# Performance work log

Hardware: AMD Instinct MI355X
Metric: run time of the kernel (lower is better)

The kernel has to match this reference:

```python
import jax, jax.numpy as jnp
import numpy as np
import math

B, L, D = 4, 4096, 64

def setup_inputs() -> dict:
    key = jax.random.key(0)
    kq, kk, kv = jax.random.split(key, 3)
    q = jax.random.normal(kq, (B, L, D), dtype=jnp.float32)
    k = jax.random.normal(kk, (B, L, D), dtype=jnp.float32)
    v = jax.random.normal(kv, (B, L, D), dtype=jnp.float32)
    return {"q": q, "k": k, "v": v}

def reference(q, k, v):
    d_model = k.shape[-1]
    # score[b,i,j] = <q_i, k_j> / sqrt(d)   -> [B, L, L]
    score = jnp.einsum('bid,bjd->bij', q, k) / math.sqrt(d_model)
    attn = jax.nn.softmax(score.astype(jnp.float32), axis=-1)
    # Faithful to source: output = (v^T @ attn)^T = attn^T @ v
    # output[b,j,d] = sum_i attn[b,i,j] * v[b,i,d]
    out = jnp.einsum('bij,bid->bjd', attn, v)
    return out
```

## Files before the change

### kernel.cpp

```cpp
#include <hip/hip_runtime.h>
#include <hip/hip_bf16.h>

#define LQ 4096
#define DD 64
#define NB 4
#define NTOT ((size_t)NB * LQ * DD)
#define NROW ((size_t)NB * LQ)

typedef __attribute__((ext_vector_type(4))) float f32x4;
typedef __attribute__((ext_vector_type(8))) short short8;
typedef __attribute__((ext_vector_type(4))) short short4v;
typedef __attribute__((ext_vector_type(2))) unsigned int uint2v;
typedef __attribute__((ext_vector_type(4))) unsigned short ushort4v;

static __device__ __forceinline__ unsigned short f2bf(float x) {
  __hip_bfloat16 h = __float2bfloat16(x);
  return __builtin_bit_cast(unsigned short, h);
}
static __device__ __forceinline__ float bf2f(unsigned short u) {
  unsigned int v = ((unsigned int)u) << 16;
  return __builtin_bit_cast(float, v);
}
static __device__ __forceinline__ float ex2(float x) { return __builtin_amdgcn_exp2f(x); }

static __device__ __forceinline__ f32x4 mfma16(short4v a, short4v b, f32x4 c) {
#if __has_builtin(__builtin_amdgcn_mfma_f32_16x16x16bf16_1k)
  return __builtin_amdgcn_mfma_f32_16x16x16bf16_1k(a, b, c, 0, 0, 0);
#else
  asm volatile("v_mfma_f32_16x16x16_bf16 %0, %1, %2, %0"
               : "+v"(c) : "v"(a), "v"(b));
  return c;
#endif
}

static __device__ __forceinline__ void gl_lds16(const unsigned short* g, unsigned short* l) {
  __builtin_amdgcn_global_load_lds(
      (const __attribute__((address_space(1))) unsigned int*)g,
      (__attribute__((address_space(3))) unsigned int*)l, 16, 0, 0);
}

#define C1 0.18033688011112042f

__global__ __launch_bounds__(256) void prep_kernel(
    const float* __restrict__ q, const float* __restrict__ k,
    const float* __restrict__ v,
    unsigned short* __restrict__ Qb, unsigned short* __restrict__ Kb,
    unsigned short* __restrict__ Vb)
{
  const int arr = blockIdx.x >> 9;
  const size_t off = (((size_t)(blockIdx.x & 511)) * 256 + threadIdx.x) * 8;
  const float* s = arr == 0 ? q : arr == 1 ? k : v;
  unsigned short* d = arr == 0 ? Qb : arr == 1 ? Kb : Vb;
  const f32x4 x0 = *(const f32x4*)(s + off);
  const f32x4 x1 = *(const f32x4*)(s + off + 4);
  ushort4v o0 = { f2bf(x0[0]), f2bf(x0[1]), f2bf(x0[2]), f2bf(x0[3]) };
  ushort4v o1 = { f2bf(x1[0]), f2bf(x1[1]), f2bf(x1[2]), f2bf(x1[3]) };
  *(ushort4v*)(d + off) = o0;
  *(ushort4v*)(d + off + 4) = o1;
}

__global__ __launch_bounds__(256, 2) void stats_kernel(
    const unsigned short* __restrict__ Qb, const unsigned short* __restrict__ Kb,
    float* __restrict__ part_ls)
{
  __shared__ __align__(16) unsigned short stK[3][2048];
  const int bx = blockIdx.x;
  const int jc = bx & 7, it = (bx >> 3) & 15, b = bx >> 7;
  const int tid = threadIdx.x, w = tid >> 6, lane = tid & 63;
  const int l15 = lane & 15, g = lane >> 4;
  const int i0 = it * 256 + w * 64;
  const int jbase = jc * 512;
  const unsigned short* Kbase = Kb + (size_t)b * LQ * DD;

  short8 aq[4][2];
#pragma unroll
  for (int is = 0; is < 4; ++is)
#pragma unroll
    for (int kh = 0; kh < 2; ++kh)
      aq[is][kh] = *(const short8*)(Qb + ((size_t)b * LQ + i0 + is * 16 + l15) * DD + kh * 32 + g * 8);

  float ls[4][4];
#pragma unroll
  for (int is = 0; is < 4; ++is)
#pragma unroll
    for (int qq = 0; qq < 4; ++qq) ls[is][qq] = 0.f;

  const int srow = w * 8 + (lane >> 3);
  const int scol = ((lane & 7) ^ (lane >> 3)) << 3;

  gl_lds16(Kbase + (size_t)(jbase + srow) * DD + scol, &stK[0][w * 512]);
  gl_lds16(Kbase + (size_t)(jbase + 32 + srow) * DD + scol, &stK[1][w * 512]);
  asm volatile("s_waitcnt vmcnt(1)" ::: "memory");
  __builtin_amdgcn_s_barrier();

  for (int itr = 0; itr < 16; ++itr) {
    const int cur = itr % 3;
    const int tn = (itr + 2 < 16) ? itr + 2 : 15;
    gl_lds16(Kbase + (size_t)(jbase + tn * 32 + srow) * DD + scol, &stK[(itr + 2) % 3][w * 512]);

    short8 kf[2][2];
#pragma unroll
    for (int jsub = 0; jsub < 2; ++jsub)
#pragma unroll
      for (int kh = 0; kh < 2; ++kh) {
        const int row = jsub * 16 + l15;
        kf[jsub][kh] = *(const short8*)(&stK[cur][row * 64 + (((kh * 4 + g) ^ (l15 & 7)) << 3)]);
      }
#pragma unroll
    for (int is = 0; is < 4; ++is)
#pragma unroll
      for (int jsub = 0; jsub < 2; ++jsub) {
        f32x4 tt = __builtin_amdgcn_mfma_f32_16x16x32_bf16(
            aq[is][0], kf[jsub][0], (f32x4){0.f, 0.f, 0.f, 0.f}, 0, 0, 0);
        tt = __builtin_amdgcn_mfma_f32_16x16x32_bf16(aq[is][1], kf[jsub][1], tt, 0, 0, 0);
#pragma unroll
        for (int qq = 0; qq < 4; ++qq) ls[is][qq] += ex2(tt[qq] * C1);
      }
    asm volatile("s_waitcnt vmcnt(1)" ::: "memory");
    __builtin_amdgcn_s_barrier();
  }
#pragma unroll
  for (int mask = 1; mask <= 8; mask <<= 1)
#pragma unroll
    for (int is = 0; is < 4; ++is)
#pragma unroll
      for (int qq = 0; qq < 4; ++qq) ls[is][qq] += __shfl_xor(ls[is][qq], mask, 64);
  if (l15 == 0) {
#pragma unroll
    for (int is = 0; is < 4; ++is)
#pragma unroll
      for (int qq = 0; qq < 4; ++qq)
        part_ls[(size_t)jc * NROW + b * LQ + i0 + is * 16 + g * 4 + qq] = ls[is][qq];
  }
}

__global__ __launch_bounds__(256) void combine_kernel(
    const float* __restrict__ part_ls, const unsigned short* __restrict__ Vb,
    unsigned short* __restrict__ Vs)
{
  const size_t base = ((size_t)blockIdx.x * 256 + threadIdx.x) * 8;
  const int r = (int)(base >> 6);
  float l = 0.f;
#pragma unroll
  for (int jc = 0; jc < 8; ++jc) l += part_ls[(size_t)jc * NROW + r];
  const float s = 1.0f / l;
  const ushort4v a = *(const ushort4v*)(Vb + base);
  const ushort4v c = *(const ushort4v*)(Vb + base + 4);
  ushort4v oa = { f2bf(bf2f(a[0]) * s), f2bf(bf2f(a[1]) * s),
                  f2bf(bf2f(a[2]) * s), f2bf(bf2f(a[3]) * s) };
  ushort4v oc = { f2bf(bf2f(c[0]) * s), f2bf(bf2f(c[1]) * s),
                  f2bf(bf2f(c[2]) * s), f2bf(bf2f(c[3]) * s) };
  *(ushort4v*)(Vs + base) = oa;
  *(ushort4v*)(Vs + base + 4) = oc;
}

__global__ __launch_bounds__(1024, 4) void attn_out_kernel(
    const unsigned short* __restrict__ Qb, const unsigned short* __restrict__ Kb,
    const unsigned short* __restrict__ Vs, float* __restrict__ out)
{
  __shared__ __align__(16) unsigned short stage[16][2][2048];

  const int bx = blockIdx.x;
  const int jt = bx & 63;
  const int b  = bx >> 6;
  const int tid = threadIdx.x, w = tid >> 6, lane = tid & 63;
  const int p = w >> 1, sub = w & 1;
  const int l15 = lane & 15, g = lane >> 4;
  const int j0 = jt * 64 + sub * 32;

  const unsigned short* Qbase = Qb + (size_t)b * LQ * DD;
  const unsigned short* Vbase = Vs + (size_t)b * LQ * DD;

  short8 ka[2][2];
#pragma unroll
  for (int jsl = 0; jsl < 2; ++jsl)
#pragma unroll
    for (int kh = 0; kh < 2; ++kh)
      ka[jsl][kh] = *(const short8*)(Kb + ((size_t)b * LQ + j0 + jsl * 16 + l15) * DD + kh * 32 + g * 8);

  f32x4 acc[2][4];
#pragma unroll
  for (int jsl = 0; jsl < 2; ++jsl)
#pragma unroll
    for (int ds = 0; ds < 4; ++ds) acc[jsl][ds] = (f32x4){0.f, 0.f, 0.f, 0.f};

  const int ibase = p * 512;
  const int qrow = lane >> 3;
  const int qcol = ((lane & 7) ^ (lane >> 3)) << 3;
  const int vgr = ((lane & 31) >> 3) * 4 + ((lane >> 1) & 3);
  const int vdc = (lane >> 5) * 16 + (lane & 1) * 8;

  const unsigned sbyte = (unsigned)(size_t)&stage[w][0][0];

#define STAGE(BUF, I0) do { \
    _Pragma("unroll") \
    for (int kk = 0; kk < 2; ++kk) { \
      gl_lds16(Qbase + (size_t)((I0) + kk * 8 + qrow) * DD + qcol, &stage[w][BUF][kk * 512]); \
      gl_lds16(Vbase + (size_t)((I0) + vgr) * DD + kk * 32 + vdc, &stage[w][BUF][1024 + kk * 512]); \
    } \
  } while (0)

  STAGE(0, ibase);
  STAGE(1, ibase + 16);

  for (int itr = 0; itr < 32; ++itr) {
    const int cur = itr & 1;
    if (itr < 31) asm volatile("s_waitcnt vmcnt(4)" ::: "memory");
    else          asm volatile("s_waitcnt vmcnt(0)" ::: "memory");

    short8 qf[2];
#pragma unroll
    for (int kh = 0; kh < 2; ++kh)
      qf[kh] = *(const short8*)(&stage[w][cur][l15 * 64 + (((kh * 4 + g) ^ (l15 & 7)) << 3)]);

    unsigned long long v0, v1, v2, v3;
    const unsigned av = sbyte + cur * 4096 + 2048 + g * 128 + l15 * 8;
    asm volatile(
        "ds_read_b64_tr_b16 %0, %4\n\t"
        "ds_read_b64_tr_b16 %1, %4 offset:512\n\t"
        "ds_read_b64_tr_b16 %2, %4 offset:1024\n\t"
        "ds_read_b64_tr_b16 %3, %4 offset:1536\n\t"
        "s_waitcnt lgkmcnt(0)"
        : "=&v"(v0), "=&v"(v1), "=&v"(v2), "=&v"(v3)
        : "v"(av) : "memory");
    short4v vf[4];
    vf[0] = __builtin_bit_cast(short4v, v0);
    vf[1] = __builtin_bit_cast(short4v, v1);
    vf[2] = __builtin_bit_cast(short4v, v2);
    vf[3] = __builtin_bit_cast(short4v, v3);

    if (itr + 2 < 32) STAGE(cur, ibase + (itr + 2) * 16);

    __builtin_amdgcn_s_setprio(1);
#pragma unroll
    for (int jsl = 0; jsl < 2; ++jsl) {
      f32x4 tt = __builtin_amdgcn_mfma_f32_16x16x32_bf16(
          qf[0], ka[jsl][0], (f32x4){0.f, 0.f, 0.f, 0.f}, 0, 0, 0);
      tt = __builtin_amdgcn_mfma_f32_16x16x32_bf16(qf[1], ka[jsl][1], tt, 0, 0, 0);
      const unsigned a0 = __builtin_bit_cast(unsigned, ex2(tt[0] * C1)) + 0x8000u;
      const unsigned a1 = __builtin_bit_cast(unsigned, ex2(tt[1] * C1)) + 0x8000u;
      const unsigned a2 = __builtin_bit_cast(unsigned, ex2(tt[2] * C1)) + 0x8000u;
      const unsigned a3 = __builtin_bit_cast(unsigned, ex2(tt[3] * C1)) + 0x8000u;
      uint2v uu;
      uu[0] = __builtin_amdgcn_perm(a1, a0, 0x07060302u);
      uu[1] = __builtin_amdgcn_perm(a3, a2, 0x07060302u);
      const short4v pa = __builtin_bit_cast(short4v, uu);
      acc[jsl][0] = mfma16(pa, vf[0], acc[jsl][0]);
      acc[jsl][1] = mfma16(pa, vf[1], acc[jsl][1]);
      acc[jsl][2] = mfma16(pa, vf[2], acc[jsl][2]);
      acc[jsl][3] = mfma16(pa, vf[3], acc[jsl][3]);
    }
    __builtin_amdgcn_s_setprio(0);
  }
#undef STAGE

  __syncthreads();
  float* red = (float*)&stage[0][0][0];
#pragma unroll
  for (int jsl = 0; jsl < 2; ++jsl)
#pragma unroll
    for (int ds = 0; ds < 4; ++ds)
#pragma unroll
      for (int qq = 0; qq < 4; ++qq)
        red[w * 2048 + (jsl * 16 + g * 4 + qq) * 64 + ds * 16 + l15] = acc[jsl][ds][qq];
  __syncthreads();
  {
    float* op = out + ((size_t)b * LQ + jt * 64) * DD;
#pragma unroll
    for (int rr = 0; rr < 4; ++rr) {
      const int r = w * 4 + rr;
      const int sr = r >> 5, rl = r & 31;
      float s = 0.f;
#pragma unroll
      for (int pp = 0; pp < 8; ++pp)
        s += red[(pp * 2 + sr) * 2048 + rl * 64 + lane];
      op[r * 64 + lane] = s;
    }
  }
}

extern "C" void kernel_launch(void* const* d_in, const int* in_sizes, int n_in,
                              void* d_out, int out_size, void* d_ws, size_t ws_size,
                              hipStream_t stream) {
  const float* q = (const float*)d_in[0];
  const float* k = (const float*)d_in[1];
  const float* v = (const float*)d_in[2];

  unsigned short* Qb = (unsigned short*)d_ws;
  unsigned short* Kb = Qb + NTOT;
  unsigned short* Vb = Kb + NTOT;
  unsigned short* Vs = Vb + NTOT;
  float* part_ls = (float*)(Vs + NTOT);
  float* outp = (float*)d_out;

  prep_kernel<<<1536, 256, 0, stream>>>(q, k, v, Qb, Kb, Vb);
  stats_kernel<<<NB * 16 * 8, 256, 0, stream>>>(Qb, Kb, part_ls);
  combine_kernel<<<512, 256, 0, stream>>>(part_ls, Vb, Vs);
  attn_out_kernel<<<NB * 64, 1024, 0, stream>>>(Qb, Kb, Vs, outp);
}
```

Measured before the change: 60.80 us.

## Pre-swizzle Q/K/V into MFMA fragment layout and load directly to registers

The prep and combine kernels now write Q, K and scaled V in a fragment-major layout, so each lane's MFMA operand is one contiguous 16-byte global load. The stats and attention kernels drop the LDS staging, swizzling and transpose reads, and prefetch fragments straight into registers with a 3-deep ring. V is now read from fp32 and scaled in combine, which removes a separate bf16 V copy. Stats uses 16 j-chunks and both main kernels remap block indices to interleave batches. The cost is more registers held per wave, with no LDS reuse of Q/V across the waves of a block.

```diff
diff --git a/kernel.cpp b/kernel.cpp
--- a/kernel.cpp
+++ b/kernel.cpp
@@ -6,6 +6,7 @@
 #define NB 4
 #define NTOT ((size_t)NB * LQ * DD)
 #define NROW ((size_t)NB * LQ)
+#define NJC 16
 
 typedef __attribute__((ext_vector_type(4))) float f32x4;
 typedef __attribute__((ext_vector_type(8))) short short8;
@@ -16,10 +17,6 @@
 static __device__ __forceinline__ unsigned short f2bf(float x) {
   __hip_bfloat16 h = __float2bfloat16(x);
   return __builtin_bit_cast(unsigned short, h);
-}
-static __device__ __forceinline__ float bf2f(unsigned short u) {
-  unsigned int v = ((unsigned int)u) << 16;
-  return __builtin_bit_cast(float, v);
 }
 static __device__ __forceinline__ float ex2(float x) { return __builtin_amdgcn_exp2f(x); }
 
@@ -33,91 +30,105 @@
 #endif
 }
 
-static __device__ __forceinline__ void gl_lds16(const unsigned short* g, unsigned short* l) {
-  __builtin_amdgcn_global_load_lds(
-      (const __attribute__((address_space(1))) unsigned int*)g,
-      (__attribute__((address_space(3))) unsigned int*)l, 16, 0, 0);
-}
-
 #define C1 0.18033688011112042f
+
 
 __global__ __launch_bounds__(256) void prep_kernel(
     const float* __restrict__ q, const float* __restrict__ k,
-    const float* __restrict__ v,
-    unsigned short* __restrict__ Qb, unsigned short* __restrict__ Kb,
-    unsigned short* __restrict__ Vb)
+    unsigned short* __restrict__ Qf, unsigned short* __restrict__ Kf)
 {
-  const int arr = blockIdx.x >> 9;
-  const size_t off = (((size_t)(blockIdx.x & 511)) * 256 + threadIdx.x) * 8;
-  const float* s = arr == 0 ? q : arr == 1 ? k : v;
-  unsigned short* d = arr == 0 ? Qb : arr == 1 ? Kb : Vb;
-  const f32x4 x0 = *(const f32x4*)(s + off);
-  const f32x4 x1 = *(const f32x4*)(s + off + 4);
-  ushort4v o0 = { f2bf(x0[0]), f2bf(x0[1]), f2bf(x0[2]), f2bf(x0[3]) };
-  ushort4v o1 = { f2bf(x1[0]), f2bf(x1[1]), f2bf(x1[2]), f2bf(x1[3]) };
-  *(ushort4v*)(d + off) = o0;
-  *(ushort4v*)(d + off + 4) = o1;
-}
-
-__global__ __launch_bounds__(256, 2) void stats_kernel(
-    const unsigned short* __restrict__ Qb, const unsigned short* __restrict__ Kb,
+  __shared__ __align__(16) unsigned short tile[64][72];
+  const int bx = blockIdx.x;
+  const int b = bx >> 6, s = bx & 63;
+  const int tid = threadIdx.x;
+  const int r = tid >> 2, c0 = (tid & 3) << 4;
+  const int w = tid >> 6, lane = tid & 63;
+  const int l15 = lane & 15, g = lane >> 4;
+  const size_t rowbase = ((size_t)b * LQ + s * 64 + r) * DD + c0;
+  const size_t bbase = (size_t)b * LQ * DD;
+
+#pragma unroll
+  for (int arr = 0; arr < 2; ++arr) {
+    const float* src = arr ? k : q;
+    unsigned short* dst = arr ? Kf : Qf;
+    ushort4v o[4];
+#pragma unroll
+    for (int e = 0; e < 4; ++e) {
+      const f32x4 x = *(const f32x4*)(src + rowbase + e * 4);
+      o[e] = (ushort4v){ f2bf(x[0]), f2bf(x[1]), f2bf(x[2]), f2bf(x[3]) };
+    }
+    if (arr) __syncthreads();
+#pragma unroll
+    for (int e = 0; e < 4; ++e) *(ushort4v*)(&tile[r][c0 + e * 4]) = o[e];
+    __syncthreads();
+    const int T = s * 4 + w;
+#pragma unroll
+    for (int kh = 0; kh < 2; ++kh) {
+      const unsigned short* pp = &tile[w * 16 + l15][kh * 32 + g * 8];
+      const ushort4v lo = *(const ushort4v*)pp;
+      const ushort4v hi = *(const ushort4v*)(pp + 4);
+      unsigned short* od = dst + bbase + (((size_t)T * 2 + kh) * 64 + lane) * 8;
+      *(ushort4v*)od = lo;
+      *(ushort4v*)(od + 4) = hi;
+    }
+  }
+}
+
+__global__ __launch_bounds__(256) void stats_kernel(
+    const unsigned short* __restrict__ Qf, const unsigned short* __restrict__ Kf,
     float* __restrict__ part_ls)
 {
-  __shared__ __align__(16) unsigned short stK[3][2048];
   const int bx = blockIdx.x;
-  const int jc = bx & 7, it = (bx >> 3) & 15, b = bx >> 7;
+  const int x = bx & 7, kk = bx >> 3;
+  const int b = x >> 1;
+  const int jc = ((x & 1) << 3) + (kk >> 4);
+  const int it = kk & 15;
   const int tid = threadIdx.x, w = tid >> 6, lane = tid & 63;
   const int l15 = lane & 15, g = lane >> 4;
-  const int i0 = it * 256 + w * 64;
-  const int jbase = jc * 512;
-  const unsigned short* Kbase = Kb + (size_t)b * LQ * DD;
+  const size_t bbase = (size_t)b * LQ * DD;
+  const unsigned short* Qp = Qf + bbase;
+  const unsigned short* Kp = Kf + bbase;
 
   short8 aq[4][2];
 #pragma unroll
   for (int is = 0; is < 4; ++is)
 #pragma unroll
+    for (int kh = 0; kh < 2; ++kh) {
+      const int T = it * 16 + w * 4 + is;
+      aq[is][kh] = *(const short8*)(Qp + (((size_t)T * 2 + kh) * 64 + lane) * 8);
+    }
+
+  float ls[4][4];
+#pragma unroll
+  for (int is = 0; is < 4; ++is)
+#pragma unroll
+    for (int qq = 0; qq < 4; ++qq) ls[is][qq] = 0.f;
+
+  const int J0 = jc * 16;
+  short8 kf[3][2];
+#pragma unroll
+  for (int pb = 0; pb < 2; ++pb)
+#pragma unroll
     for (int kh = 0; kh < 2; ++kh)
-      aq[is][kh] = *(const short8*)(Qb + ((size_t)b * LQ + i0 + is * 16 + l15) * DD + kh * 32 + g * 8);
-
-  float ls[4][4];
-#pragma unroll
-  for (int is = 0; is < 4; ++is)
-#pragma unroll
-    for (int qq = 0; qq < 4; ++qq) ls[is][qq] = 0.f;
-
-  const int srow = w * 8 + (lane >> 3);
-  const int scol = ((lane & 7) ^ (lane >> 3)) << 3;
-
-  gl_lds16(Kbase + (size_t)(jbase + srow) * DD + scol, &stK[0][w * 512]);
-  gl_lds16(Kbase + (size_t)(jbase + 32 + srow) * DD + scol, &stK[1][w * 512]);
-  asm volatile("s_waitcnt vmcnt(1)" ::: "memory");
-  __builtin_amdgcn_s_barrier();
-
+      kf[pb][kh] = *(const short8*)(Kp + (((size_t)(J0 + pb) * 2 + kh) * 64 + lane) * 8);
+
+#pragma unroll
   for (int itr = 0; itr < 16; ++itr) {
-    const int cur = itr % 3;
-    const int tn = (itr + 2 < 16) ? itr + 2 : 15;
-    gl_lds16(Kbase + (size_t)(jbase + tn * 32 + srow) * DD + scol, &stK[(itr + 2) % 3][w * 512]);
-
-    short8 kf[2][2];
-#pragma unroll
-    for (int jsub = 0; jsub < 2; ++jsub)
-#pragma unroll
-      for (int kh = 0; kh < 2; ++kh) {
-        const int row = jsub * 16 + l15;
-        kf[jsub][kh] = *(const short8*)(&stK[cur][row * 64 + (((kh * 4 + g) ^ (l15 & 7)) << 3)]);
-      }
-#pragma unroll
-    for (int is = 0; is < 4; ++is)
-#pragma unroll
-      for (int jsub = 0; jsub < 2; ++jsub) {
-        f32x4 tt = __builtin_amdgcn_mfma_f32_16x16x32_bf16(
-            aq[is][0], kf[jsub][0], (f32x4){0.f, 0.f, 0.f, 0.f}, 0, 0, 0);
-        tt = __builtin_amdgcn_mfma_f32_16x16x32_bf16(aq[is][1], kf[jsub][1], tt, 0, 0, 0);
-#pragma unroll
-        for (int qq = 0; qq < 4; ++qq) ls[is][qq] += ex2(tt[qq] * C1);
-      }
-    asm volatile("s_waitcnt vmcnt(1)" ::: "memory");
-    __builtin_amdgcn_s_barrier();
+    const int buf = itr % 3;
+    if (itr + 2 < 16) {
+      const int nb2 = (itr + 2) % 3;
+#pragma unroll
+      for (int kh = 0; kh < 2; ++kh)
+        kf[nb2][kh] = *(const short8*)(Kp + (((size_t)(J0 + itr + 2) * 2 + kh) * 64 + lane) * 8);
+    }
+#pragma unroll
+    for (int is = 0; is < 4; ++is) {
+      f32x4 tt = __builtin_amdgcn_mfma_f32_16x16x32_bf16(
+          aq[is][0], kf[buf][0], (f32x4){0.f, 0.f, 0.f, 0.f}, 0, 0, 0);
+      tt = __builtin_amdgcn_mfma_f32_16x16x32_bf16(aq[is][1], kf[buf][1], tt, 0, 0, 0);
+#pragma unroll
+      for (int qq = 0; qq < 4; ++qq) ls[is][qq] += ex2(tt[qq] * C1);
+    }
   }
 #pragma unroll
   for (int mask = 1; mask <= 8; mask <<= 1)
@@ -127,116 +138,128 @@
       for (int qq = 0; qq < 4; ++qq) ls[is][qq] += __shfl_xor(ls[is][qq], mask, 64);
   if (l15 == 0) {
 #pragma unroll
-    for (int is = 0; is < 4; ++is)
+    for (int is = 0; is < 4; ++is) {
+      const int T = it * 16 + w * 4 + is;
 #pragma unroll
       for (int qq = 0; qq < 4; ++qq)
-        part_ls[(size_t)jc * NROW + b * LQ + i0 + is * 16 + g * 4 + qq] = ls[is][qq];
+        part_ls[(size_t)jc * NROW + b * LQ + T * 16 + g * 4 + qq] = ls[is][qq];
+    }
   }
 }
 
 __global__ __launch_bounds__(256) void combine_kernel(
-    const float* __restrict__ part_ls, const unsigned short* __restrict__ Vb,
-    unsigned short* __restrict__ Vs)
+    const float* __restrict__ part_ls, const float* __restrict__ v,
+    unsigned short* __restrict__ Vf)
 {
-  const size_t base = ((size_t)blockIdx.x * 256 + threadIdx.x) * 8;
-  const int r = (int)(base >> 6);
+  __shared__ __align__(16) unsigned short tile[64][72];
+  const int bx = blockIdx.x;
+  const int b = bx >> 6, s = bx & 63;
+  const int tid = threadIdx.x;
+  const int r = tid >> 2, c0 = (tid & 3) << 4;
+  const int w = tid >> 6, lane = tid & 63;
+  const int l15 = lane & 15, g = lane >> 4;
+  const int row = b * LQ + s * 64 + r;
+
   float l = 0.f;
 #pragma unroll
-  for (int jc = 0; jc < 8; ++jc) l += part_ls[(size_t)jc * NROW + r];
-  const float s = 1.0f / l;
-  const ushort4v a = *(const ushort4v*)(Vb + base);
-  const ushort4v c = *(const ushort4v*)(Vb + base + 4);
-  ushort4v oa = { f2bf(bf2f(a[0]) * s), f2bf(bf2f(a[1]) * s),
-                  f2bf(bf2f(a[2]) * s), f2bf(bf2f(a[3]) * s) };
-  ushort4v oc = { f2bf(bf2f(c[0]) * s), f2bf(bf2f(c[1]) * s),
-                  f2bf(bf2f(c[2]) * s), f2bf(bf2f(c[3]) * s) };
-  *(ushort4v*)(Vs + base) = oa;
-  *(ushort4v*)(Vs + base + 4) = oc;
-}
-
-__global__ __launch_bounds__(1024, 4) void attn_out_kernel(
-    const unsigned short* __restrict__ Qb, const unsigned short* __restrict__ Kb,
-    const unsigned short* __restrict__ Vs, float* __restrict__ out)
+  for (int jc = 0; jc < NJC; ++jc) l += part_ls[(size_t)jc * NROW + row];
+  const float sc = 1.0f / l;
+
+  const size_t rowbase = (size_t)row * DD + c0;
+#pragma unroll
+  for (int e = 0; e < 4; ++e) {
+    const f32x4 xv = *(const f32x4*)(v + rowbase + e * 4);
+    ushort4v o = { f2bf(xv[0] * sc), f2bf(xv[1] * sc),
+                   f2bf(xv[2] * sc), f2bf(xv[3] * sc) };
+    *(ushort4v*)(&tile[r][c0 + e * 4]) = o;
+  }
+  __syncthreads();
+  const int T = s * 4 + w;
+  const size_t bbase = (size_t)b * LQ * DD;
+#pragma unroll
+  for (int dp = 0; dp < 2; ++dp) {
+    ushort4v lo, hi;
+#pragma unroll
+    for (int c = 0; c < 4; ++c) {
+      lo[c] = tile[w * 16 + g * 4 + c][(2 * dp) * 16 + l15];
+      hi[c] = tile[w * 16 + g * 4 + c][(2 * dp + 1) * 16 + l15];
+    }
+    unsigned short* od = Vf + bbase + (((size_t)T * 2 + dp) * 64 + lane) * 8;
+    *(ushort4v*)od = lo;
+    *(ushort4v*)(od + 4) = hi;
+  }
+}
+
+__global__ __launch_bounds__(1024) void attn_out_kernel(
+    const unsigned short* __restrict__ Qf, const unsigned short* __restrict__ Kf,
+    const unsigned short* __restrict__ Vf, float* __restrict__ out)
 {
-  __shared__ __align__(16) unsigned short stage[16][2][2048];
+  __shared__ float red[16 * 2048];
 
   const int bx = blockIdx.x;
-  const int jt = bx & 63;
-  const int b  = bx >> 6;
+  const int x = bx & 7;
+  const int b = x >> 1;
+  const int jt = ((x & 1) << 5) + (bx >> 3);
   const int tid = threadIdx.x, w = tid >> 6, lane = tid & 63;
   const int p = w >> 1, sub = w & 1;
   const int l15 = lane & 15, g = lane >> 4;
-  const int j0 = jt * 64 + sub * 32;
-
-  const unsigned short* Qbase = Qb + (size_t)b * LQ * DD;
-  const unsigned short* Vbase = Vs + (size_t)b * LQ * DD;
+
+  const size_t bbase = (size_t)b * LQ * DD;
+  const unsigned short* Qp = Qf + bbase;
+  const unsigned short* Kp = Kf + bbase;
+  const unsigned short* Vp = Vf + bbase;
 
   short8 ka[2][2];
 #pragma unroll
   for (int jsl = 0; jsl < 2; ++jsl)
 #pragma unroll
+    for (int kh = 0; kh < 2; ++kh) {
+      const int JT = jt * 4 + sub * 2 + jsl;
+      ka[jsl][kh] = *(const short8*)(Kp + (((size_t)JT * 2 + kh) * 64 + lane) * 8);
+    }
+
+  f32x4 acc[2][4];
+#pragma unroll
+  for (int jsl = 0; jsl < 2; ++jsl)
+#pragma unroll
+    for (int ds = 0; ds < 4; ++ds) acc[jsl][ds] = (f32x4){0.f, 0.f, 0.f, 0.f};
+
+  const int T0 = p * 32;
+  short8 qb[3][2], vb[3][2];
+#pragma unroll
+  for (int pb = 0; pb < 2; ++pb) {
+#pragma unroll
     for (int kh = 0; kh < 2; ++kh)
-      ka[jsl][kh] = *(const short8*)(Kb + ((size_t)b * LQ + j0 + jsl * 16 + l15) * DD + kh * 32 + g * 8);
-
-  f32x4 acc[2][4];
-#pragma unroll
-  for (int jsl = 0; jsl < 2; ++jsl)
-#pragma unroll
-    for (int ds = 0; ds < 4; ++ds) acc[jsl][ds] = (f32x4){0.f, 0.f, 0.f, 0.f};
-
-  const int ibase = p * 512;
-  const int qrow = lane >> 3;
-  const int qcol = ((lane & 7) ^ (lane >> 3)) << 3;
-  const int vgr = ((lane & 31) >> 3) * 4 + ((lane >> 1) & 3);
-  const int vdc = (lane >> 5) * 16 + (lane & 1) * 8;
-
-  const unsigned sbyte = (unsigned)(size_t)&stage[w][0][0];
-
-#define STAGE(BUF, I0) do { \
-    _Pragma("unroll") \
-    for (int kk = 0; kk < 2; ++kk) { \
-      gl_lds16(Qbase + (size_t)((I0) + kk * 8 + qrow) * DD + qcol, &stage[w][BUF][kk * 512]); \
-      gl_lds16(Vbase + (size_t)((I0) + vgr) * DD + kk * 32 + vdc, &stage[w][BUF][1024 + kk * 512]); \
-    } \
-  } while (0)
-
-  STAGE(0, ibase);
-  STAGE(1, ibase + 16);
-
+      qb[pb][kh] = *(const short8*)(Qp + (((size_t)(T0 + pb) * 2 + kh) * 64 + lane) * 8);
+#pragma unroll
+    for (int dp = 0; dp < 2; ++dp)
+      vb[pb][dp] = *(const short8*)(Vp + (((size_t)(T0 + pb) * 2 + dp) * 64 + lane) * 8);
+  }
+
+#pragma unroll
   for (int itr = 0; itr < 32; ++itr) {
-    const int cur = itr & 1;
-    if (itr < 31) asm volatile("s_waitcnt vmcnt(4)" ::: "memory");
-    else          asm volatile("s_waitcnt vmcnt(0)" ::: "memory");
-
-    short8 qf[2];
-#pragma unroll
-    for (int kh = 0; kh < 2; ++kh)
-      qf[kh] = *(const short8*)(&stage[w][cur][l15 * 64 + (((kh * 4 + g) ^ (l15 & 7)) << 3)]);
-
-    unsigned long long v0, v1, v2, v3;
-    const unsigned av = sbyte + cur * 4096 + 2048 + g * 128 + l15 * 8;
-    asm volatile(
-        "ds_read_b64_tr_b16 %0, %4\n\t"
-        "ds_read_b64_tr_b16 %1, %4 offset:512\n\t"
-        "ds_read_b64_tr_b16 %2, %4 offset:1024\n\t"
-        "ds_read_b64_tr_b16 %3, %4 offset:1536\n\t"
-        "s_waitcnt lgkmcnt(0)"
-        : "=&v"(v0), "=&v"(v1), "=&v"(v2), "=&v"(v3)
-        : "v"(av) : "memory");
-    short4v vf[4];
-    vf[0] = __builtin_bit_cast(short4v, v0);
-    vf[1] = __builtin_bit_cast(short4v, v1);
-    vf[2] = __builtin_bit_cast(short4v, v2);
-    vf[3] = __builtin_bit_cast(short4v, v3);
-
-    if (itr + 2 < 32) STAGE(cur, ibase + (itr + 2) * 16);
+    const int buf = itr % 3;
+    if (itr + 2 < 32) {
+      const int nb2 = (itr + 2) % 3;
+      const int Tn = T0 + itr + 2;
+#pragma unroll
+      for (int kh = 0; kh < 2; ++kh)
+        qb[nb2][kh] = *(const short8*)(Qp + (((size_t)Tn * 2 + kh) * 64 + lane) * 8);
+#pragma unroll
+      for (int dp = 0; dp < 2; ++dp)
+        vb[nb2][dp] = *(const short8*)(Vp + (((size_t)Tn * 2 + dp) * 64 + lane) * 8);
+    }
+
+    union VU { short8 s8; short4v s4[2]; } vu0, vu1;
+    vu0.s8 = vb[buf][0];
+    vu1.s8 = vb[buf][1];
 
     __builtin_amdgcn_s_setprio(1);
 #pragma unroll
     for (int jsl = 0; jsl < 2; ++jsl) {
       f32x4 tt = __builtin_amdgcn_mfma_f32_16x16x32_bf16(
-          qf[0], ka[jsl][0], (f32x4){0.f, 0.f, 0.f, 0.f}, 0, 0, 0);
-      tt = __builtin_amdgcn_mfma_f32_16x16x32_bf16(qf[1], ka[jsl][1], tt, 0, 0, 0);
+          qb[buf][0], ka[jsl][0], (f32x4){0.f, 0.f, 0.f, 0.f}, 0, 0, 0);
+      tt = __builtin_amdgcn_mfma_f32_16x16x32_bf16(qb[buf][1], ka[jsl][1], tt, 0, 0, 0);
       const unsigned a0 = __builtin_bit_cast(unsigned, ex2(tt[0] * C1)) + 0x8000u;
       const unsigned a1 = __builtin_bit_cast(unsigned, ex2(tt[1] * C1)) + 0x8000u;
       const unsigned a2 = __builtin_bit_cast(unsigned, ex2(tt[2] * C1)) + 0x8000u;
@@ -245,17 +268,15 @@
       uu[0] = __builtin_amdgcn_perm(a1, a0, 0x07060302u);
       uu[1] = __builtin_amdgcn_perm(a3, a2, 0x07060302u);
       const short4v pa = __builtin_bit_cast(short4v, uu);
-      acc[jsl][0] = mfma16(pa, vf[0], acc[jsl][0]);
-      acc[jsl][1] = mfma16(pa, vf[1], acc[jsl][1]);
-      acc[jsl][2] = mfma16(pa, vf[2], acc[jsl][2]);
-      acc[jsl][3] = mfma16(pa, vf[3], acc[jsl][3]);
+      acc[jsl][0] = mfma16(pa, vu0.s4[0], acc[jsl][0]);
+      acc[jsl][1] = mfma16(pa, vu0.s4[1], acc[jsl][1]);
+      acc[jsl][2] = mfma16(pa, vu1.s4[0], acc[jsl][2]);
+      acc[jsl][3] = mfma16(pa, vu1.s4[1], acc[jsl][3]);
     }
     __builtin_amdgcn_s_setprio(0);
   }
-#undef STAGE
 
   __syncthreads();
-  float* red = (float*)&stage[0][0][0];
 #pragma unroll
   for (int jsl = 0; jsl < 2; ++jsl)
 #pragma unroll
@@ -286,15 +307,14 @@
   const float* k = (const float*)d_in[1];
   const float* v = (const float*)d_in[2];
 
-  unsigned short* Qb = (unsigned short*)d_ws;
-  unsigned short* Kb = Qb + NTOT;
-  unsigned short* Vb = Kb + NTOT;
-  unsigned short* Vs = Vb + NTOT;
-  float* part_ls = (float*)(Vs + NTOT);
+  unsigned short* Qf = (unsigned short*)d_ws;
+  unsigned short* Kf = Qf + NTOT;
+  unsigned short* Vf = Kf + NTOT;
+  float* part_ls = (float*)(Vf + NTOT);
   float* outp = (float*)d_out;
 
-  prep_kernel<<<1536, 256, 0, stream>>>(q, k, v, Qb, Kb, Vb);
-  stats_kernel<<<NB * 16 * 8, 256, 0, stream>>>(Qb, Kb, part_ls);
-  combine_kernel<<<512, 256, 0, stream>>>(part_ls, Vb, Vs);
-  attn_out_kernel<<<NB * 64, 1024, 0, stream>>>(Qb, Kb, Vs, outp);
-}
+  prep_kernel<<<NB * 64, 256, 0, stream>>>(q, k, Qf, Kf);
+  stats_kernel<<<1024, 256, 0, stream>>>(Qf, Kf, part_ls);
+  combine_kernel<<<NB * 64, 256, 0, stream>>>(part_ls, v, Vf);
+  attn_out_kernel<<<256, 1024, 0, stream>>>(Qf, Kf, Vf, outp);
+}
```

New measurement: 52.47 us. -13.7%, faster.
